# Optimization experiments

Measured on AMD Instinct MI355X. Metric: run time of the kernel, lower is better.

## Reference

```python
import jax, jax.numpy as jnp
import numpy as np

EMB_DIM = 1024
NUM_HEADS = 16
HEAD_DIM = EMB_DIM // NUM_HEADS
SEQ_LEN = 2048
BATCH = 2


def setup_inputs() -> dict:
    key = jax.random.key(0)
    k1, k2, k3 = jax.random.split(key, 3)
    scale = 1.0 / np.sqrt(EMB_DIM)
    x = jax.random.normal(k1, (BATCH, SEQ_LEN, EMB_DIM), dtype=jnp.float32)
    w_qkv = jax.random.normal(k2, (EMB_DIM, 3 * EMB_DIM), dtype=jnp.float32) * scale
    w_proj = jax.random.normal(k3, (EMB_DIM, EMB_DIM), dtype=jnp.float32) * scale
    b_proj = jnp.zeros((EMB_DIM,), dtype=jnp.float32)
    return {"x": x, "w_qkv": w_qkv, "w_proj": w_proj, "b_proj": b_proj}


def reference(x, w_qkv, w_proj, b_proj):
    B, T, E = x.shape
    qkv = x @ w_qkv                                   # [B, T, 3E]
    q, k, v = jnp.split(qkv, 3, axis=-1)
    # -> [B, H, T, D]
    def heads(t):
        return t.reshape(B, T, NUM_HEADS, HEAD_DIM).transpose(0, 2, 1, 3)
    q, k, v = heads(q), heads(k), heads(v)
    att = jnp.einsum("bhqd,bhkd->bhqk", q, k) / np.sqrt(HEAD_DIM).astype(x.dtype)
    causal = jnp.tril(jnp.ones((T, T), dtype=bool))   # True = keep
    att = jnp.where(causal, att, jnp.array(-jnp.inf, dtype=att.dtype))
    att = jax.nn.softmax(att, axis=-1)
    out = jnp.einsum("bhqk,bhkd->bhqd", att, v)       # [B, H, T, D]
    out = out.transpose(0, 2, 1, 3).reshape(B, T, E)
    return out @ w_proj + b_proj
```

## Files before the change

### kernel.cpp

```cpp
#include <hip/hip_runtime.h>

typedef __bf16 bf16x8 __attribute__((ext_vector_type(8)));
typedef __bf16 bf16x4 __attribute__((ext_vector_type(4)));
typedef float  f32x4  __attribute__((ext_vector_type(4)));
typedef float  f32x16 __attribute__((ext_vector_type(16)));
typedef unsigned u32x2 __attribute__((ext_vector_type(2)));
typedef unsigned u32x4 __attribute__((ext_vector_type(4)));

#define T_SEQ 2048
#define NH    16
#define HD    64
#define EMB   1024
#define BATCH 2
#define QSCALE 0.18033688f

__device__ __forceinline__ void gload_lds16(const void* g, void* lds) {
  __builtin_amdgcn_global_load_lds(
      (__attribute__((address_space(1))) void*)(g),
      (__attribute__((address_space(3))) void*)(lds), 16, 0, 0);
}

__device__ __forceinline__ f32x16 mfma32(bf16x8 a, bf16x8 b, f32x16 c) {
  return __builtin_amdgcn_mfma_f32_32x32x16_bf16(a, b, c, 0, 0, 0);
}

__device__ __forceinline__ f32x4 mfma16(bf16x8 a, bf16x8 b, f32x4 c) {
  return __builtin_amdgcn_mfma_f32_16x16x32_bf16(a, b, c, 0, 0, 0);
}

__device__ __forceinline__ unsigned cvtpk(float lo, float hi) {
  unsigned short a = __builtin_bit_cast(unsigned short, (__bf16)lo);
  unsigned short b = __builtin_bit_cast(unsigned short, (__bf16)hi);
  return (unsigned)a | ((unsigned)b << 16);
}

__global__ __launch_bounds__(256) void cvt_bf16(const float* __restrict__ in,
                                                __bf16* __restrict__ out, int n) {
  int i = (blockIdx.x * 256 + threadIdx.x) * 8;
  if (i >= n) return;
  f32x4 a = *(const f32x4*)(in + i);
  f32x4 b = *(const f32x4*)(in + i + 4);
  bf16x8 v;
  v[0] = (__bf16)a[0]; v[1] = (__bf16)a[1]; v[2] = (__bf16)a[2]; v[3] = (__bf16)a[3];
  v[4] = (__bf16)b[0]; v[5] = (__bf16)b[1]; v[6] = (__bf16)b[2]; v[7] = (__bf16)b[3];
  *(bf16x8*)(out + i) = v;
}

__global__ __launch_bounds__(256) void transpose_cvt(const float* __restrict__ in,
                                                     __bf16* __restrict__ out,
                                                     int rows, int cols) {
  __shared__ float tile[32][33];
  int c0 = blockIdx.x * 32, r0 = blockIdx.y * 32;
  int tx = threadIdx.x & 31, ty = threadIdx.x >> 5;
#pragma unroll
  for (int j = 0; j < 32; j += 8)
    tile[ty + j][tx] = in[(size_t)(r0 + ty + j) * cols + c0 + tx];
  __syncthreads();
#pragma unroll
  for (int j = 0; j < 32; j += 8)
    out[(size_t)(c0 + ty + j) * rows + r0 + tx] = (__bf16)tile[tx][ty + j];
}

template <int MODE>
__global__ __launch_bounds__(256) void gemm_bt(
    const __bf16* __restrict__ A, const __bf16* __restrict__ Bt, int K,
    __bf16* __restrict__ Qo, __bf16* __restrict__ Ko, __bf16* __restrict__ Vt,
    const float* __restrict__ bias, float* __restrict__ Cout) {
  __shared__ alignas(16) __bf16 sA[3][128 * 32];
  __shared__ alignas(16) __bf16 sB[3][128 * 32];
  const int tid = threadIdx.x;
  const int w = tid >> 6, l = tid & 63;
  const int m0 = blockIdx.y * 128, n0 = blockIdx.x * 128;
  const int lc = l & 15, lu = l >> 4;
  const int mw = (w >> 1) * 64, nw = (w & 1) * 64;
  const int rA = l >> 2;
  const int usw = (((l & 3) ^ ((rA >> 1) & 3))) * 8;
  const int rsw = (lu ^ ((lc >> 1) & 3)) * 8;

  f32x4 acc[4][4] = {};

  auto stage = [&](int buf, int kt) {
#pragma unroll
    for (int i = 0; i < 2; ++i) {
      int rr = (w * 2 + i) * 16;
      gload_lds16(A  + (size_t)(m0 + rr + rA) * K + kt + usw, &sA[buf][rr * 32]);
      gload_lds16(Bt + (size_t)(n0 + rr + rA) * K + kt + usw, &sB[buf][rr * 32]);
    }
  };

  const int NT = K >> 5;
  stage(0, 0);
  stage(1, 32);

  int bi = 0;
  for (int i = 0; i < NT; ++i) {
    if (i == NT - 1) { asm volatile("s_waitcnt vmcnt(0)" ::: "memory"); }
    else             { asm volatile("s_waitcnt vmcnt(4)" ::: "memory"); }
    __builtin_amdgcn_s_barrier();
    __builtin_amdgcn_sched_barrier(0);

    if (i + 2 < NT) {
      int bs = bi + 2; if (bs >= 3) bs -= 3;
      stage(bs, (i + 2) * 32);
    }

    bf16x8 af[4], bfr[4];
#pragma unroll
    for (int f = 0; f < 4; ++f) {
      af[f]  = *(const bf16x8*)(&sA[bi][(mw + f * 16 + lc) * 32 + rsw]);
      bfr[f] = *(const bf16x8*)(&sB[bi][(nw + f * 16 + lc) * 32 + rsw]);
    }
#pragma unroll
    for (int mf = 0; mf < 4; ++mf)
#pragma unroll
      for (int nf = 0; nf < 4; ++nf)
        acc[mf][nf] = mfma16(af[mf], bfr[nf], acc[mf][nf]);

    if (++bi >= 3) bi = 0;
  }

#pragma unroll
  for (int mf = 0; mf < 4; ++mf) {
#pragma unroll
    for (int nf = 0; nf < 4; ++nf) {
#pragma unroll
      for (int r = 0; r < 4; ++r) {
        int mg = m0 + mw + mf * 16 + lu * 4 + r;
        int ng = n0 + nw + nf * 16 + lc;
        float v = acc[mf][nf][r];
        if (MODE == 0) {
          int part = ng >> 10;
          int h = (ng >> 6) & 15;
          int d = ng & 63;
          int b = mg >> 11;
          int t = mg & 2047;
          if (part == 0) {
            Qo[(((size_t)(b * NH + h)) * T_SEQ + t) * HD + d] = (__bf16)(v * QSCALE);
          } else if (part == 1) {
            Ko[(((size_t)(b * NH + h)) * T_SEQ + t) * HD + d] = (__bf16)v;
          } else {
            Vt[(((size_t)(b * NH + h)) * HD + d) * T_SEQ + t] = (__bf16)v;
          }
        } else {
          Cout[(size_t)mg * EMB + ng] = v + bias[ng];
        }
      }
    }
  }
}

__global__ __launch_bounds__(256) void gemm_proj(
    const __bf16* __restrict__ A, const __bf16* __restrict__ Bt, int K,
    const float* __restrict__ bias, float* __restrict__ Cout) {
  __shared__ alignas(16) __bf16 sA[3][128 * 32];
  __shared__ alignas(16) __bf16 sB[3][64 * 32];
  const int tid = threadIdx.x;
  const int w = tid >> 6, l = tid & 63;
  const int m0 = blockIdx.y * 128, n0 = blockIdx.x * 64;
  const int lc = l & 15, lu = l >> 4;
  const int mw = (w >> 1) * 64, nw = (w & 1) * 32;
  const int rA = l >> 2;
  const int usw = (((l & 3) ^ ((rA >> 1) & 3))) * 8;
  const int rsw = (lu ^ ((lc >> 1) & 3)) * 8;

  f32x4 acc[4][2] = {};

  auto stage = [&](int buf, int kt) {
#pragma unroll
    for (int i = 0; i < 2; ++i) {
      int rr = (w * 2 + i) * 16;
      gload_lds16(A + (size_t)(m0 + rr + rA) * K + kt + usw, &sA[buf][rr * 32]);
    }
    gload_lds16(Bt + (size_t)(n0 + w * 16 + rA) * K + kt + usw,
                &sB[buf][w * 16 * 32]);
  };

  const int NT = K >> 5;
  stage(0, 0);
  stage(1, 32);

  int bi = 0;
  for (int i = 0; i < NT; ++i) {
    if (i == NT - 1) { asm volatile("s_waitcnt vmcnt(0)" ::: "memory"); }
    else             { asm volatile("s_waitcnt vmcnt(3)" ::: "memory"); }
    __builtin_amdgcn_s_barrier();
    __builtin_amdgcn_sched_barrier(0);

    if (i + 2 < NT) {
      int bs = bi + 2; if (bs >= 3) bs -= 3;
      stage(bs, (i + 2) * 32);
    }

    bf16x8 af[4], bfr[2];
#pragma unroll
    for (int f = 0; f < 4; ++f)
      af[f] = *(const bf16x8*)(&sA[bi][(mw + f * 16 + lc) * 32 + rsw]);
#pragma unroll
    for (int f = 0; f < 2; ++f)
      bfr[f] = *(const bf16x8*)(&sB[bi][(nw + f * 16 + lc) * 32 + rsw]);
#pragma unroll
    for (int mf = 0; mf < 4; ++mf)
#pragma unroll
      for (int nf = 0; nf < 2; ++nf)
        acc[mf][nf] = mfma16(af[mf], bfr[nf], acc[mf][nf]);

    if (++bi >= 3) bi = 0;
  }

#pragma unroll
  for (int mf = 0; mf < 4; ++mf)
#pragma unroll
    for (int nf = 0; nf < 2; ++nf)
#pragma unroll
      for (int r = 0; r < 4; ++r) {
        int mg = m0 + mw + mf * 16 + lu * 4 + r;
        int ng = n0 + nw + nf * 16 + lc;
        Cout[(size_t)mg * EMB + ng] = acc[mf][nf][r] + bias[ng];
      }
}

__device__ __forceinline__ void cmask32(f32x16& s0, int k0, int hi, int q) {
#pragma unroll
  for (int r = 0; r < 16; ++r) {
    int kk = k0 + 4 * hi + (r & 3) + 8 * (r >> 2);
    if (kk > q) s0[r] = -1e30f;
  }
}

__device__ __forceinline__ void softmax_pack32(
    f32x16& s0, f32x16& o0, f32x16& o1,
    float& m, float& ls, u32x4 (&pf)[2]) {
  float mx[8];
#pragma unroll
  for (int r = 0; r < 8; ++r) mx[r] = fmaxf(s0[r], s0[r + 8]);
#pragma unroll
  for (int st = 4; st > 0; st >>= 1)
#pragma unroll
    for (int r = 0; r < 8; ++r) if (r < st) mx[r] = fmaxf(mx[r], mx[r + st]);
  float pmax = fmaxf(mx[0], __shfl_xor(mx[0], 32));
  if (!__all(pmax <= m + 8.0f)) {
    float mn = fmaxf(m, pmax);
    float al = __builtin_amdgcn_exp2f(m - mn);
    m = mn;
    ls *= al;
#pragma unroll
    for (int r = 0; r < 16; ++r) { o0[r] *= al; o1[r] *= al; }
  }
  float ps = 0.f;
  f32x16 p;
#pragma unroll
  for (int r = 0; r < 16; ++r) { p[r] = __builtin_amdgcn_exp2f(s0[r] - m); ps += p[r]; }
  ps += __shfl_xor(ps, 32);
  ls += ps;
#pragma unroll
  for (int kh = 0; kh < 2; ++kh) {
    unsigned c01 = cvtpk(p[kh * 8 + 0], p[kh * 8 + 1]);
    unsigned c23 = cvtpk(p[kh * 8 + 2], p[kh * 8 + 3]);
    unsigned c45 = cvtpk(p[kh * 8 + 4], p[kh * 8 + 5]);
    unsigned c67 = cvtpk(p[kh * 8 + 6], p[kh * 8 + 7]);
    u32x2 a = __builtin_amdgcn_permlane32_swap(c01, c45, false, false);
    u32x2 c = __builtin_amdgcn_permlane32_swap(c23, c67, false, false);
    u32x4 r; r[0] = a[0]; r[1] = c[0]; r[2] = a[1]; r[3] = c[1];
    pf[kh] = r;
  }
}

__device__ __forceinline__ void dump_state(float* mo, float* mm, int reg, int l,
                                           const f32x16& o0, const f32x16& o1,
                                           float m, float ls) {
  float* po = mo + reg * 2048 + l;
#pragma unroll
  for (int r = 0; r < 16; ++r) { po[r * 64] = o0[r]; po[(16 + r) * 64] = o1[r]; }
  mm[reg * 128 + l] = m;
  mm[reg * 128 + 64 + l] = ls;
}

__device__ __forceinline__ void merge_write(const float* mo, const float* mm,
                                            int reg, int l, int hi,
                                            const f32x16& o0, const f32x16& o1,
                                            float m, float ls,
                                            __bf16* O, size_t rowbase) {
  float m1 = mm[reg * 128 + l];
  float l1 = mm[reg * 128 + 64 + l];
  float mn = fmaxf(m, m1);
  float a0 = __builtin_amdgcn_exp2f(m - mn);
  float a1 = __builtin_amdgcn_exp2f(m1 - mn);
  float inv = 1.f / (ls * a0 + l1 * a1);
  const float* po = mo + reg * 2048 + l;
#pragma unroll
  for (int dt = 0; dt < 2; ++dt) {
    const f32x16& ov = dt ? o1 : o0;
#pragma unroll
    for (int rg = 0; rg < 4; ++rg) {
      bf16x4 vv;
#pragma unroll
      for (int j = 0; j < 4; ++j) {
        int r = rg * 4 + j;
        float oth = po[(dt * 16 + r) * 64];
        vv[j] = (__bf16)((ov[r] * a0 + oth * a1) * inv);
      }
      int d = dt * 32 + rg * 8 + 4 * hi;
      *(bf16x4*)(O + rowbase + d) = vv;
    }
  }
}

__global__ __launch_bounds__(512, 4) void attn(
    const __bf16* __restrict__ Q,
    const __bf16* __restrict__ K,
    const __bf16* __restrict__ Vt,
    __bf16* __restrict__ O) {
  __shared__ alignas(16) __bf16 sKV[12][32 * 64];
  __shared__ alignas(16) float mls[4 * 2 * 64];

  const int x = blockIdx.x, bh = blockIdx.y;
  const int tid = threadIdx.x, w = tid >> 6, l = tid & 63;
  const int lq = l & 31, hi = l >> 5;
  const int c  = w >> 2;
  const int st = (w >> 1) & 1;
  const int gc = w & 1;
  const int kind = w >> 2, sp = (w >> 1) & 1, shf = w & 1;

  const __bf16* Qh = Q + (size_t)bh * T_SEQ * HD;
  const __bf16* Kh = K + (size_t)bh * T_SEQ * HD;
  const __bf16* Vh = Vt + (size_t)bh * HD * T_SEQ;

  const int C = (c == 0) ? (31 - x) : x;
  const int q0 = C * 64 + st * 32;
  const int diagT = 2 * C + st;
  const int nsup = 32 - x;

  bf16x8 qf[4];
#pragma unroll
  for (int dc = 0; dc < 4; ++dc)
    qf[dc] = *(const bf16x8*)(Qh + (size_t)(q0 + lq) * HD + dc * 16 + hi * 8);

  f32x16 o0 = {}, o1 = {};
  float m = -1e30f, ls = 0.f;

  const int r8 = l >> 3;
  const int kswz = ((l & 7) ^ r8) * 8;
  const int r4 = l >> 2;
  const int vswz = ((l & 3) ^ (r4 & 3)) * 8;

  auto stage = [&](int buf, int ss) {
    int t = 2 * ss + sp;
    int k0s = t * 32;
    if (kind == 0) {
      __bf16* dst = &sKV[buf * 2 + sp][shf * 16 * 64];
#pragma unroll
      for (int i = 0; i < 2; ++i)
        gload_lds16(Kh + (size_t)(k0s + shf * 16 + i * 8 + r8) * HD + kswz,
                    dst + i * 512);
    } else {
      __bf16* dst = &sKV[6 + buf * 2 + sp][shf * 32 * 32];
#pragma unroll
      for (int i = 0; i < 2; ++i)
        gload_lds16(Vh + (size_t)(shf * 32 + i * 16 + r4) * T_SEQ + k0s + vswz,
                    dst + i * 512);
    }
  };

  auto kfrag = [&](const __bf16* b, int row, int u) -> bf16x8 {
    return *(const bf16x8*)(b + row * 64 + ((u ^ (row & 7)) << 3));
  };
  auto vfrag = [&](const __bf16* b, int row, int u) -> bf16x8 {
    return *(const bf16x8*)(b + row * 32 + ((u ^ (row & 3)) << 3));
  };

  stage(0, 0);
  stage(1, 1);

  int buf = 0;
  for (int ss = 0; ss < nsup; ++ss) {
    if (ss + 1 < nsup) { asm volatile("s_waitcnt vmcnt(2)" ::: "memory"); }
    else               { asm volatile("s_waitcnt vmcnt(0)" ::: "memory"); }
    __builtin_amdgcn_s_barrier();
    __builtin_amdgcn_sched_barrier(0);

    if (ss + 2 < nsup) {
      int bs = buf + 2; if (bs >= 3) bs -= 3;
      stage(bs, ss + 2);
    }

    const int tg = 2 * ss + gc;
    if (tg <= diagT) {
      const __bf16* sKb = &sKV[buf * 2 + gc][0];
      const __bf16* sVb = &sKV[6 + buf * 2 + gc][0];
      f32x16 s = {};
#pragma unroll
      for (int dc = 0; dc < 4; ++dc)
        s = mfma32(kfrag(sKb, lq, dc * 2 + hi), qf[dc], s);
      if (tg == diagT) cmask32(s, tg * 32, hi, q0 + lq);
      u32x4 pf[2];
      softmax_pack32(s, o0, o1, m, ls, pf);
#pragma unroll
      for (int ks = 0; ks < 2; ++ks) {
        bf16x8 vf0 = vfrag(sVb, lq, ks * 2 + hi);
        bf16x8 vf1 = vfrag(sVb, 32 + lq, ks * 2 + hi);
        bf16x8 pa = __builtin_bit_cast(bf16x8, pf[ks]);
        o0 = mfma32(vf0, pa, o0);
        o1 = mfma32(vf1, pa, o1);
      }
    }
    if (++buf >= 3) buf = 0;
  }

  __syncthreads();
  float* mo = (float*)&sKV[0][0];
  const int reg = c * 2 + st;
  if (gc == 1) dump_state(mo, mls, reg, l, o0, o1, m, ls);
  __syncthreads();
  if (gc == 0) {
    const int b = bh >> 4, h = bh & 15;
    size_t row = (size_t)(b * T_SEQ + q0 + lq) * EMB + h * HD;
    merge_write(mo, mls, reg, l, hi, o0, o1, m, ls, O, row);
  }
}

extern "C" void kernel_launch(void* const* d_in, const int* in_sizes, int n_in,
                              void* d_out, int out_size, void* d_ws, size_t ws_size,
                              hipStream_t stream) {
  const float* x      = (const float*)d_in[0];
  const float* w_qkv  = (const float*)d_in[1];
  const float* w_proj = (const float*)d_in[2];
  const float* b_proj = (const float*)d_in[3];
  float* out = (float*)d_out;

  char* ws = (char*)d_ws;
  __bf16* xb     = (__bf16*)(ws);
  __bf16* wqkvT  = (__bf16*)(ws + (8u  << 20));
  __bf16* wprojT = (__bf16*)(ws + (14u << 20));
  __bf16* Qw     = (__bf16*)(ws + (16u << 20));
  __bf16* Kw     = (__bf16*)(ws + (24u << 20));
  __bf16* Vw     = (__bf16*)(ws + (32u << 20));
  __bf16* Ow     = xb;

  cvt_bf16<<<2048, 256, 0, stream>>>(x, xb, 4096 * 1024);
  transpose_cvt<<<dim3(3072 / 32, 1024 / 32), 256, 0, stream>>>(w_qkv, wqkvT, 1024, 3072);
  transpose_cvt<<<dim3(1024 / 32, 1024 / 32), 256, 0, stream>>>(w_proj, wprojT, 1024, 1024);

  gemm_bt<0><<<dim3(3072 / 128, 4096 / 128), 256, 0, stream>>>(
      xb, wqkvT, 1024, Qw, Kw, Vw, nullptr, nullptr);

  attn<<<dim3(16, BATCH * NH), 512, 0, stream>>>(Qw, Kw, Vw, Ow);

  gemm_proj<<<dim3(1024 / 64, 4096 / 128), 256, 0, stream>>>(
      Ow, wprojT, 1024, b_proj, out);
}
```

Baseline: 123.4 us.

## Split paired causal attention blocks into single-chunk blocks and vectorize Vt epilogue stores

The attention kernel used to pair a long and a short query chunk in one 512-thread block to balance causal work. It now launches one 256-thread block per 64-row query chunk, with heavy chunks scheduled first and each wave staging more K/V tiles. The aim is finer-grained scheduling and more resident blocks, at the cost of uneven per-block work and some lost K/V sharing. Separately, the QKV GEMM epilogue now writes the transposed V output as a packed 4-element bf16 vector per lane instead of four scalar strided stores.

```diff
diff --git a/kernel.cpp b/kernel.cpp
--- a/kernel.cpp
+++ b/kernel.cpp
@@ -123,26 +123,36 @@
   for (int mf = 0; mf < 4; ++mf) {
 #pragma unroll
     for (int nf = 0; nf < 4; ++nf) {
-#pragma unroll
-      for (int r = 0; r < 4; ++r) {
-        int mg = m0 + mw + mf * 16 + lu * 4 + r;
+      if (MODE == 0) {
         int ng = n0 + nw + nf * 16 + lc;
-        float v = acc[mf][nf][r];
-        if (MODE == 0) {
-          int part = ng >> 10;
-          int h = (ng >> 6) & 15;
-          int d = ng & 63;
-          int b = mg >> 11;
-          int t = mg & 2047;
-          if (part == 0) {
-            Qo[(((size_t)(b * NH + h)) * T_SEQ + t) * HD + d] = (__bf16)(v * QSCALE);
-          } else if (part == 1) {
-            Ko[(((size_t)(b * NH + h)) * T_SEQ + t) * HD + d] = (__bf16)v;
-          } else {
-            Vt[(((size_t)(b * NH + h)) * HD + d) * T_SEQ + t] = (__bf16)v;
-          }
+        int part = ng >> 10;
+        int h = (ng >> 6) & 15;
+        int d = ng & 63;
+        int mg0 = m0 + mw + mf * 16 + lu * 4;
+        int b = mg0 >> 11;
+        int t0 = mg0 & 2047;
+        if (part == 2) {
+          bf16x4 v4;
+#pragma unroll
+          for (int r = 0; r < 4; ++r) v4[r] = (__bf16)acc[mf][nf][r];
+          *(bf16x4*)(Vt + ((size_t)(b * NH + h) * HD + d) * T_SEQ + t0) = v4;
+        } else if (part == 0) {
+#pragma unroll
+          for (int r = 0; r < 4; ++r)
+            Qo[((size_t)(b * NH + h) * T_SEQ + t0 + r) * HD + d] =
+                (__bf16)(acc[mf][nf][r] * QSCALE);
         } else {
-          Cout[(size_t)mg * EMB + ng] = v + bias[ng];
+#pragma unroll
+          for (int r = 0; r < 4; ++r)
+            Ko[((size_t)(b * NH + h) * T_SEQ + t0 + r) * HD + d] =
+                (__bf16)acc[mf][nf][r];
+        }
+      } else {
+#pragma unroll
+        for (int r = 0; r < 4; ++r) {
+          int mg = m0 + mw + mf * 16 + lu * 4 + r;
+          int ng = n0 + nw + nf * 16 + lc;
+          Cout[(size_t)mg * EMB + ng] = acc[mf][nf][r] + bias[ng];
         }
       }
     }
@@ -305,30 +315,27 @@
   }
 }
 
-__global__ __launch_bounds__(512, 4) void attn(
+__global__ __launch_bounds__(256, 3) void attn(
     const __bf16* __restrict__ Q,
     const __bf16* __restrict__ K,
     const __bf16* __restrict__ Vt,
     __bf16* __restrict__ O) {
   __shared__ alignas(16) __bf16 sKV[12][32 * 64];
-  __shared__ alignas(16) float mls[4 * 2 * 64];
-
-  const int x = blockIdx.x, bh = blockIdx.y;
+  __shared__ alignas(16) float mls[2 * 128];
+
+  const int C = 31 - blockIdx.x, bh = blockIdx.y;
   const int tid = threadIdx.x, w = tid >> 6, l = tid & 63;
   const int lq = l & 31, hi = l >> 5;
-  const int c  = w >> 2;
-  const int st = (w >> 1) & 1;
-  const int gc = w & 1;
-  const int kind = w >> 2, sp = (w >> 1) & 1, shf = w & 1;
+  const int st = w >> 1, gc = w & 1;
+  const int kind = w >> 1, sp = w & 1;
 
   const __bf16* Qh = Q + (size_t)bh * T_SEQ * HD;
   const __bf16* Kh = K + (size_t)bh * T_SEQ * HD;
   const __bf16* Vh = Vt + (size_t)bh * HD * T_SEQ;
 
-  const int C = (c == 0) ? (31 - x) : x;
   const int q0 = C * 64 + st * 32;
   const int diagT = 2 * C + st;
-  const int nsup = 32 - x;
+  const int nsup = C + 1;
 
   bf16x8 qf[4];
 #pragma unroll
@@ -344,20 +351,17 @@
   const int vswz = ((l & 3) ^ (r4 & 3)) * 8;
 
   auto stage = [&](int buf, int ss) {
-    int t = 2 * ss + sp;
-    int k0s = t * 32;
+    int k0s = (2 * ss + sp) * 32;
     if (kind == 0) {
-      __bf16* dst = &sKV[buf * 2 + sp][shf * 16 * 64];
-#pragma unroll
-      for (int i = 0; i < 2; ++i)
-        gload_lds16(Kh + (size_t)(k0s + shf * 16 + i * 8 + r8) * HD + kswz,
-                    dst + i * 512);
+      __bf16* dst = &sKV[buf * 2 + sp][0];
+#pragma unroll
+      for (int i = 0; i < 4; ++i)
+        gload_lds16(Kh + (size_t)(k0s + i * 8 + r8) * HD + kswz, dst + i * 512);
     } else {
-      __bf16* dst = &sKV[6 + buf * 2 + sp][shf * 32 * 32];
-#pragma unroll
-      for (int i = 0; i < 2; ++i)
-        gload_lds16(Vh + (size_t)(shf * 32 + i * 16 + r4) * T_SEQ + k0s + vswz,
-                    dst + i * 512);
+      __bf16* dst = &sKV[6 + buf * 2 + sp][0];
+#pragma unroll
+      for (int i = 0; i < 4; ++i)
+        gload_lds16(Vh + (size_t)(i * 16 + r4) * T_SEQ + k0s + vswz, dst + i * 512);
     }
   };
 
@@ -369,11 +373,11 @@
   };
 
   stage(0, 0);
-  stage(1, 1);
+  if (nsup > 1) stage(1, 1);
 
   int buf = 0;
   for (int ss = 0; ss < nsup; ++ss) {
-    if (ss + 1 < nsup) { asm volatile("s_waitcnt vmcnt(2)" ::: "memory"); }
+    if (ss + 1 < nsup) { asm volatile("s_waitcnt vmcnt(4)" ::: "memory"); }
     else               { asm volatile("s_waitcnt vmcnt(0)" ::: "memory"); }
     __builtin_amdgcn_s_barrier();
     __builtin_amdgcn_sched_barrier(0);
@@ -408,13 +412,12 @@
 
   __syncthreads();
   float* mo = (float*)&sKV[0][0];
-  const int reg = c * 2 + st;
-  if (gc == 1) dump_state(mo, mls, reg, l, o0, o1, m, ls);
+  if (gc == 1) dump_state(mo, mls, st, l, o0, o1, m, ls);
   __syncthreads();
   if (gc == 0) {
     const int b = bh >> 4, h = bh & 15;
     size_t row = (size_t)(b * T_SEQ + q0 + lq) * EMB + h * HD;
-    merge_write(mo, mls, reg, l, hi, o0, o1, m, ls, O, row);
+    merge_write(mo, mls, st, l, hi, o0, o1, m, ls, O, row);
   }
 }
 
@@ -443,7 +446,7 @@
   gemm_bt<0><<<dim3(3072 / 128, 4096 / 128), 256, 0, stream>>>(
       xb, wqkvT, 1024, Qw, Kw, Vw, nullptr, nullptr);
 
-  attn<<<dim3(16, BATCH * NH), 512, 0, stream>>>(Qw, Kw, Vw, Ow);
+  attn<<<dim3(32, BATCH * NH), 256, 0, stream>>>(Qw, Kw, Vw, Ow);
 
   gemm_proj<<<dim3(1024 / 64, 4096 / 128), 256, 0, stream>>>(
       Ow, wprojT, 1024, b_proj, out);
```

New measurement: 139.5 us. +13.1%, slower.
